# Optimization experiments

Hardware: AMD Instinct MI355X
Metric: run time of the kernel (lower is better)

Reference implementation:

```python
import jax, jax.numpy as jnp
import numpy as np

N = 204800   # total item nodes across the ragged batch
B = 4096     # number of session graphs
D = 256      # item_dim == output_dim
TAO = 1.0


def setup_inputs() -> dict:
    key = jax.random.key(0)
    k1, k2, k3, k4, k5, k6 = jax.random.split(key, 6)
    ifeat = jax.random.normal(k1, (N, D), dtype=jnp.float32)
    seg_ids = jnp.sort(jax.random.randint(k2, (N,), 0, B)).astype(jnp.int64)
    s = 1.0 / np.sqrt(D)
    Wu = jax.random.uniform(k3, (D, D), jnp.float32, -s, s)   # fc_u weight (no bias)
    Wv = jax.random.uniform(k4, (D, D), jnp.float32, -s, s)   # fc_v weight
    bv = jax.random.uniform(k5, (D,), jnp.float32, -s, s)     # fc_v bias
    we = jax.random.uniform(k6, (D,), jnp.float32, -s, s)     # fc_e weight -> scalar per node
    return {"ifeat": ifeat, "Wu": Wu, "Wv": Wv, "bv": bv, "we": we, "seg_ids": seg_ids}


def reference(ifeat, Wu, Wv, bv, we, seg_ids):
    seg = seg_ids.astype(jnp.int32)
    # anchor: segment mean of ifeat (pooling_type='imean')
    counts = jax.ops.segment_sum(jnp.ones((N,), ifeat.dtype), seg, num_segments=B)
    seg_sum = jax.ops.segment_sum(ifeat, seg, num_segments=B)          # [B, D]
    anchor = seg_sum / jnp.maximum(counts, 1.0)[:, None]               # [B, D]
    # attention logits
    ifeat_u = ifeat @ Wu.T                                             # [N, D]
    feat_v = (anchor @ Wv.T + bv)[seg]                                 # broadcast_nodes -> [N, D]
    e = jax.nn.sigmoid(ifeat_u + feat_v) @ we                          # [N]
    e = e / TAO
    # segment softmax over nodes of each session
    e_max = jax.ops.segment_max(e, seg, num_segments=B)                # [B]
    ex = jnp.exp(e - e_max[seg])                                       # [N]
    denom = jax.ops.segment_sum(ex, seg, num_segments=B)               # [B]
    alpha = ex / denom[seg]                                            # [N]
    # weighted segment sum
    rst = jax.ops.segment_sum(ifeat * alpha[:, None], seg, num_segments=B)  # [B, D]
    return jnp.concatenate([rst, anchor], axis=1)                      # [B, 2D]
```

## Files before the change

### kernel.cpp

```cpp
#include <hip/hip_runtime.h>
#include <hip/hip_bf16.h>

#define DD 256
#define NN 204800
#define SB 4096

typedef __attribute__((ext_vector_type(8))) short bf16x8;
typedef __attribute__((ext_vector_type(4))) float f32x4;

__device__ __forceinline__ unsigned short f2bf(float x) {
    union { float f; unsigned u; } v; v.f = x;
    unsigned r = v.u + 0x7FFF + ((v.u >> 16) & 1);
    return (unsigned short)(r >> 16);
}
__device__ __forceinline__ float bf2f(unsigned short h) {
    union { unsigned u; float f; } v; v.u = ((unsigned)h) << 16;
    return v.f;
}

__global__ void k_prep(const int* __restrict__ seg, const float* __restrict__ Wu,
                       int* __restrict__ seg_start, unsigned short* __restrict__ wub) {
    int blk = blockIdx.x, t = threadIdx.x;
    if (blk < 17) {
        int b = blk * 256 + t;
        if (b > SB) return;
        int lo = 0, hi = NN;
        while (lo < hi) {
            int mid = (lo + hi) >> 1;
            if (seg[mid] < b) lo = mid + 1; else hi = mid;
        }
        seg_start[b] = lo;
    } else {
        int o = (blk - 17) * 256 + t;
        int j    = o & 7;
        int colr = (o >> 3) & 15;
        int kg   = (o >> 7) & 3;
        int kt   = (o >> 9) & 7;
        int dt   = o >> 12;
        wub[o] = f2bf(Wu[(dt * 16 + colr) * DD + kt * 32 + kg * 8 + j]);
    }
}

__global__ __launch_bounds__(256) void k_anchor(
    const float* __restrict__ ifeat, const int* __restrict__ seg_start,
    unsigned short* __restrict__ xbf, float* __restrict__ anc_ws,
    float* __restrict__ out)
{
    __shared__ float ancp[4][DD];
    int b = blockIdx.x, t = threadIdx.x;
    int rg = t >> 6, ct = (t & 63) * 4;
    int s0 = seg_start[b], s1 = seg_start[b + 1];
    int C = s1 - s0;
    f32x4 asum = {0.f, 0.f, 0.f, 0.f};
    for (int i0 = 0; i0 < C; i0 += 4) {
        int i = i0 + rg;
        if (i < C) {
            const f32x4 v = __builtin_nontemporal_load(
                (const f32x4*)&ifeat[(size_t)(s0 + i) * DD + ct]);
            asum.x += v.x; asum.y += v.y; asum.z += v.z; asum.w += v.w;
            ushort4 h;
            h.x = f2bf(v.x); h.y = f2bf(v.y); h.z = f2bf(v.z); h.w = f2bf(v.w);
            *(ushort4*)&xbf[(size_t)(s0 + i) * DD + ct] = h;
        }
    }
    *(f32x4*)&ancp[rg][ct] = asum;
    __syncthreads();
    float a = ancp[0][t] + ancp[1][t] + ancp[2][t] + ancp[3][t];
    float m = a / fmaxf((float)C, 1.f);
    anc_ws[b * DD + t] = m;
    out[(size_t)b * 2 * DD + DD + t] = m;
}

__global__ void k_featv(const float* __restrict__ anc_ws, const float* __restrict__ Wv,
                        const float* __restrict__ bv, float* __restrict__ feat_v) {
    int b0 = blockIdx.x * 16;
    int d = threadIdx.x;
    __shared__ float anc[16][DD];
    #pragma unroll
    for (int r = 0; r < 16; ++r) anc[r][d] = anc_ws[(b0 + r) * DD + d];
    __syncthreads();
    float acc[16];
    float bvd = bv[d];
    #pragma unroll
    for (int r = 0; r < 16; ++r) acc[r] = bvd;
    for (int k = 0; k < DD; k += 4) {
        float4 wv4 = *(const float4*)&Wv[d * DD + k];
        #pragma unroll
        for (int r = 0; r < 16; ++r) {
            acc[r] += wv4.x * anc[r][k] + wv4.y * anc[r][k + 1]
                    + wv4.z * anc[r][k + 2] + wv4.w * anc[r][k + 3];
        }
    }
    #pragma unroll
    for (int r = 0; r < 16; ++r) feat_v[(b0 + r) * DD + d] = acc[r];
}

__global__ __launch_bounds__(256, 3) void k_e(
    const unsigned short* __restrict__ xbf,
    const unsigned short* __restrict__ wub,
    const float* __restrict__ feat_v,
    const float* __restrict__ we,
    const int* __restrict__ seg,
    float* __restrict__ e_ws)
{
    __shared__ unsigned short bsh[2][4096];
    const int t = threadIdx.x;
    const int w = t >> 6, lane = t & 63;
    const int colr = lane & 15, kg = lane >> 4;
    const int wbase = blockIdx.x * 128 + w * 32;

    bf16x8 a[2][8];
    {
        const unsigned short* ap = &xbf[(size_t)(wbase + colr) * DD + kg * 8];
        #pragma unroll
        for (int rt = 0; rt < 2; ++rt)
            #pragma unroll
            for (int kt = 0; kt < 8; ++kt)
                a[rt][kt] = *(const bf16x8*)(ap + rt * 16 * DD + kt * 32);
    }

    int sgv[2][4];
    #pragma unroll
    for (int rt = 0; rt < 2; ++rt)
        #pragma unroll
        for (int r = 0; r < 4; ++r)
            sgv[rt][r] = seg[wbase + rt * 16 + kg * 4 + r];

    float epart[2][4];
    #pragma unroll
    for (int rt = 0; rt < 2; ++rt)
        #pragma unroll
        for (int r = 0; r < 4; ++r) epart[rt][r] = 0.f;

    {
        const uint4* s = (const uint4*)&wub[t * 16];
        uint4 v0 = s[0], v1 = s[1];
        *(uint4*)&bsh[0][t * 16] = v0;
        *(uint4*)&bsh[0][t * 16 + 8] = v1;
    }
    __syncthreads();

    #pragma unroll 2
    for (int dt = 0; dt < 16; ++dt) {
        const int cur = dt & 1;
        if (dt < 15) {
            const uint4* s = (const uint4*)&wub[(dt + 1) * 4096 + t * 16];
            uint4 v0 = s[0], v1 = s[1];
            *(uint4*)&bsh[cur ^ 1][t * 16] = v0;
            *(uint4*)&bsh[cur ^ 1][t * 16 + 8] = v1;
        }

        f32x4 acc0 = (f32x4){0.f, 0.f, 0.f, 0.f};
        f32x4 acc1 = (f32x4){0.f, 0.f, 0.f, 0.f};
        #pragma unroll
        for (int kt = 0; kt < 8; ++kt) {
            bf16x8 bfr = *(const bf16x8*)&bsh[cur][kt * 512 + lane * 8];
            acc0 = __builtin_amdgcn_mfma_f32_16x16x32_bf16(a[0][kt], bfr, acc0, 0, 0, 0);
            acc1 = __builtin_amdgcn_mfma_f32_16x16x32_bf16(a[1][kt], bfr, acc1, 0, 0, 0);
        }

        const float wed = we[dt * 16 + colr];
        #pragma unroll
        for (int r = 0; r < 4; ++r) {
            float fv0 = feat_v[(size_t)sgv[0][r] * DD + dt * 16 + colr];
            float fv1 = feat_v[(size_t)sgv[1][r] * DD + dt * 16 + colr];
            float u0 = acc0[r] + fv0;
            float u1 = acc1[r] + fv1;
            epart[0][r] += wed * __builtin_amdgcn_rcpf(1.f + __expf(-u0));
            epart[1][r] += wed * __builtin_amdgcn_rcpf(1.f + __expf(-u1));
        }
        __syncthreads();
    }

    #pragma unroll
    for (int rt = 0; rt < 2; ++rt) {
        #pragma unroll
        for (int r = 0; r < 4; ++r) {
            float p = epart[rt][r];
            p += __shfl_xor(p, 1, 64);
            p += __shfl_xor(p, 2, 64);
            p += __shfl_xor(p, 4, 64);
            p += __shfl_xor(p, 8, 64);
            if (colr == 0) e_ws[wbase + rt * 16 + kg * 4 + r] = __expf(p);
        }
    }
}

__global__ __launch_bounds__(256) void k_rst(
    const unsigned short* __restrict__ xbf, const float* __restrict__ e_ws,
    const int* __restrict__ seg_start, float* __restrict__ out)
{
    int b = blockIdx.x, t = threadIdx.x;
    int s0 = seg_start[b], s1 = seg_start[b + 1];
    int C = s1 - s0;
    if (C <= 0) { out[(size_t)b * 2 * DD + t] = 0.f; return; }
    __shared__ float part[4][DD];
    __shared__ float red[4];
    __shared__ float bsum;
    int lane = t & 63, w = t >> 6;

    float s = 0.f;
    for (int i = t; i < C; i += 256) s += e_ws[s0 + i];
    #pragma unroll
    for (int off = 1; off < 64; off <<= 1) s += __shfl_xor(s, off, 64);
    if (lane == 0) red[w] = s;
    __syncthreads();
    if (t == 0) bsum = red[0] + red[1] + red[2] + red[3];
    __syncthreads();
    const float inv = 1.f / bsum;

    int rg = t >> 6, ct = (t & 63) * 4;
    f32x4 racc = {0.f, 0.f, 0.f, 0.f};
    for (int i0 = 0; i0 < C; i0 += 4) {
        int i = i0 + rg;
        if (i < C) {
            float al = e_ws[s0 + i];
            ushort4 v = *(const ushort4*)&xbf[(size_t)(s0 + i) * DD + ct];
            racc.x += al * bf2f(v.x);
            racc.y += al * bf2f(v.y);
            racc.z += al * bf2f(v.z);
            racc.w += al * bf2f(v.w);
        }
    }
    *(f32x4*)&part[rg][ct] = racc;
    __syncthreads();
    out[(size_t)b * 2 * DD + t] = (part[0][t] + part[1][t] + part[2][t] + part[3][t]) * inv;
}

extern "C" void kernel_launch(void* const* d_in, const int* in_sizes, int n_in,
                              void* d_out, int out_size, void* d_ws, size_t ws_size,
                              hipStream_t stream) {
    const float* ifeat = (const float*)d_in[0];
    const float* Wu    = (const float*)d_in[1];
    const float* Wv    = (const float*)d_in[2];
    const float* bv    = (const float*)d_in[3];
    const float* we    = (const float*)d_in[4];
    const int*   seg   = (const int*)d_in[5];
    float* out = (float*)d_out;

    char* ws = (char*)d_ws;
    int* seg_start        = (int*)ws;
    unsigned short* wub   = (unsigned short*)(ws + 32768);
    float* anc_ws         = (float*)(ws + 32768 + 131072);
    float* feat_v         = (float*)(ws + 32768 + 131072 + 4194304);
    float* e_ws           = (float*)(ws + 32768 + 131072 + 8388608);
    unsigned short* xbf   = (unsigned short*)(ws + 32768 + 131072 + 8388608 + 819200);

    k_prep<<<dim3(273), dim3(256), 0, stream>>>(seg, Wu, seg_start, wub);
    k_anchor<<<dim3(SB), dim3(256), 0, stream>>>(ifeat, seg_start, xbf, anc_ws, out);
    k_featv<<<dim3(SB / 16), dim3(256), 0, stream>>>(anc_ws, Wv, bv, feat_v);
    k_e<<<dim3(NN / 128), dim3(256), 0, stream>>>(xbf, wub, feat_v, we, seg, e_ws);
    k_rst<<<dim3(SB), dim3(256), 0, stream>>>(xbf, e_ws, seg_start, out);
}
```

Baseline: 154.7 us.

## Fuse anchor-to-feat_v projection into anchor kernel using pre-transposed Wv

Removes the separate k_featv launch and the anc_ws round trip through global memory. Each anchor block now computes its own feat_v row, reading a transposed copy of Wv (built in k_prep) so accesses are coalesced across threads. In exchange, each of the 4096 blocks re-reads the full 256KB Wv from cache instead of sharing it across 16 batches per block, which adds L2 traffic and serial tail work to the bandwidth-bound anchor kernel.

```diff
diff --git a/kernel.cpp b/kernel.cpp
--- a/kernel.cpp
+++ b/kernel.cpp
@@ -19,7 +19,9 @@
 }
 
 __global__ void k_prep(const int* __restrict__ seg, const float* __restrict__ Wu,
-                       int* __restrict__ seg_start, unsigned short* __restrict__ wub) {
+                       const float* __restrict__ Wv,
+                       int* __restrict__ seg_start, unsigned short* __restrict__ wub,
+                       float* __restrict__ wvT) {
     int blk = blockIdx.x, t = threadIdx.x;
     if (blk < 17) {
         int b = blk * 256 + t;
@@ -30,7 +32,7 @@
             if (seg[mid] < b) lo = mid + 1; else hi = mid;
         }
         seg_start[b] = lo;
-    } else {
+    } else if (blk < 273) {
         int o = (blk - 17) * 256 + t;
         int j    = o & 7;
         int colr = (o >> 3) & 15;
@@ -38,15 +40,25 @@
         int kt   = (o >> 9) & 7;
         int dt   = o >> 12;
         wub[o] = f2bf(Wu[(dt * 16 + colr) * DD + kt * 32 + kg * 8 + j]);
+    } else {
+        int idx = (blk - 273) * 1024 + t * 4;
+        int d = idx >> 8, k0 = idx & 255;
+        const float4 v = *(const float4*)&Wv[d * DD + k0];
+        wvT[(size_t)(k0 + 0) * DD + d] = v.x;
+        wvT[(size_t)(k0 + 1) * DD + d] = v.y;
+        wvT[(size_t)(k0 + 2) * DD + d] = v.z;
+        wvT[(size_t)(k0 + 3) * DD + d] = v.w;
     }
 }
 
 __global__ __launch_bounds__(256) void k_anchor(
     const float* __restrict__ ifeat, const int* __restrict__ seg_start,
-    unsigned short* __restrict__ xbf, float* __restrict__ anc_ws,
+    const float* __restrict__ wvT, const float* __restrict__ bv,
+    unsigned short* __restrict__ xbf, float* __restrict__ feat_v,
     float* __restrict__ out)
 {
     __shared__ float ancp[4][DD];
+    __shared__ float anc_s[DD];
     int b = blockIdx.x, t = threadIdx.x;
     int rg = t >> 6, ct = (t & 63) * 4;
     int s0 = seg_start[b], s1 = seg_start[b + 1];
@@ -67,32 +79,18 @@
     __syncthreads();
     float a = ancp[0][t] + ancp[1][t] + ancp[2][t] + ancp[3][t];
     float m = a / fmaxf((float)C, 1.f);
-    anc_ws[b * DD + t] = m;
+    anc_s[t] = m;
     out[(size_t)b * 2 * DD + DD + t] = m;
-}
-
-__global__ void k_featv(const float* __restrict__ anc_ws, const float* __restrict__ Wv,
-                        const float* __restrict__ bv, float* __restrict__ feat_v) {
-    int b0 = blockIdx.x * 16;
-    int d = threadIdx.x;
-    __shared__ float anc[16][DD];
-    #pragma unroll
-    for (int r = 0; r < 16; ++r) anc[r][d] = anc_ws[(b0 + r) * DD + d];
-    __syncthreads();
-    float acc[16];
-    float bvd = bv[d];
-    #pragma unroll
-    for (int r = 0; r < 16; ++r) acc[r] = bvd;
+    __syncthreads();
+    float fv = bv[t];
+    #pragma unroll 4
     for (int k = 0; k < DD; k += 4) {
-        float4 wv4 = *(const float4*)&Wv[d * DD + k];
-        #pragma unroll
-        for (int r = 0; r < 16; ++r) {
-            acc[r] += wv4.x * anc[r][k] + wv4.y * anc[r][k + 1]
-                    + wv4.z * anc[r][k + 2] + wv4.w * anc[r][k + 3];
-        }
-    }
-    #pragma unroll
-    for (int r = 0; r < 16; ++r) feat_v[(b0 + r) * DD + d] = acc[r];
+        fv += anc_s[k]     * wvT[(size_t)k * DD + t]
+            + anc_s[k + 1] * wvT[(size_t)(k + 1) * DD + t]
+            + anc_s[k + 2] * wvT[(size_t)(k + 2) * DD + t]
+            + anc_s[k + 3] * wvT[(size_t)(k + 3) * DD + t];
+    }
+    feat_v[(size_t)b * DD + t] = fv;
 }
 
 __global__ __launch_bounds__(256, 3) void k_e(
@@ -241,14 +239,13 @@
     char* ws = (char*)d_ws;
     int* seg_start        = (int*)ws;
     unsigned short* wub   = (unsigned short*)(ws + 32768);
-    float* anc_ws         = (float*)(ws + 32768 + 131072);
-    float* feat_v         = (float*)(ws + 32768 + 131072 + 4194304);
-    float* e_ws           = (float*)(ws + 32768 + 131072 + 8388608);
-    unsigned short* xbf   = (unsigned short*)(ws + 32768 + 131072 + 8388608 + 819200);
-
-    k_prep<<<dim3(273), dim3(256), 0, stream>>>(seg, Wu, seg_start, wub);
-    k_anchor<<<dim3(SB), dim3(256), 0, stream>>>(ifeat, seg_start, xbf, anc_ws, out);
-    k_featv<<<dim3(SB / 16), dim3(256), 0, stream>>>(anc_ws, Wv, bv, feat_v);
+    float* wvT            = (float*)(ws + 32768 + 131072);
+    float* feat_v         = (float*)(ws + 32768 + 131072 + 262144);
+    float* e_ws           = (float*)(ws + 32768 + 131072 + 262144 + 4194304);
+    unsigned short* xbf   = (unsigned short*)(ws + 32768 + 131072 + 262144 + 4194304 + 819200);
+
+    k_prep<<<dim3(337), dim3(256), 0, stream>>>(seg, Wu, Wv, seg_start, wub, wvT);
+    k_anchor<<<dim3(SB), dim3(256), 0, stream>>>(ifeat, seg_start, wvT, bv, xbf, feat_v, out);
     k_e<<<dim3(NN / 128), dim3(256), 0, stream>>>(xbf, wub, feat_v, we, seg, e_ws);
     k_rst<<<dim3(SB), dim3(256), 0, stream>>>(xbf, e_ws, seg_start, out);
 }
```

After: 167.2 us. +8.1%, slower.
